# Performance work log

Hardware: AMD Instinct MI355X
Metric: run time of the kernel (lower is better)

Reference implementation:

```python
import jax, jax.numpy as jnp
import numpy as np
from jax import lax

K = 3      # kernel size
PAD = 1    # padding (stride=1, dilation=1, single offset group)


def _deform_conv2d(x, off, weight, bias):
    # x: [B,C,H,W], off: [B,2*K*K,H,W] (y,x per tap), weight: [O,C,K,K], bias: [O]
    B, C, H, W = x.shape
    KK = K * K
    off = off.reshape(B, KK, 2, H, W)
    off_y, off_x = off[:, :, 0], off[:, :, 1]          # [B,KK,H,W]

    kh = jnp.repeat(jnp.arange(K, dtype=x.dtype), K)   # [KK] tap row offsets
    kw = jnp.tile(jnp.arange(K, dtype=x.dtype), K)     # [KK] tap col offsets
    py = (jnp.arange(H, dtype=x.dtype)[None, None, :, None] - PAD
          + kh[None, :, None, None] + off_y)           # [B,KK,H,W] sample rows
    px = (jnp.arange(W, dtype=x.dtype)[None, None, None, :] - PAD
          + kw[None, :, None, None] + off_x)           # [B,KK,H,W] sample cols

    y0 = jnp.floor(py); x0 = jnp.floor(px)
    wy1 = py - y0; wx1 = px - x0
    wy0 = 1.0 - wy1; wx0 = 1.0 - wx1

    bidx = jnp.arange(B)[:, None, None, None]

    def gather(iy, ix):
        # zero outside the input (torchvision semantics)
        valid = (iy >= 0) & (iy < H) & (ix >= 0) & (ix < W)
        iyc = jnp.clip(iy, 0, H - 1).astype(jnp.int32)
        ixc = jnp.clip(ix, 0, W - 1).astype(jnp.int32)
        v = x[bidx, :, iyc, ixc]                       # [B,KK,H,W,C]
        return v * valid[..., None].astype(x.dtype)

    samp = (gather(y0, x0)           * (wy0 * wx0)[..., None]
            + gather(y0, x0 + 1)     * (wy0 * wx1)[..., None]
            + gather(y0 + 1, x0)     * (wy1 * wx0)[..., None]
            + gather(y0 + 1, x0 + 1) * (wy1 * wx1)[..., None])  # [B,KK,H,W,C]

    w = weight.reshape(weight.shape[0], C, KK)          # [O,C,KK]
    out = jnp.einsum('bkhwc,ock->bohw', samp, w) + bias[None, :, None, None]
    return out


def setup_inputs() -> dict:
    key = jax.random.key(0)
    k1, k2, k3 = jax.random.split(key, 3)
    B, C, O, H, W = 4, 64, 64, 128, 128
    x = jax.random.normal(k1, (B, C, H, W), dtype=jnp.float32)
    offset_w = jax.random.normal(k2, (2 * K * K, C, 3, 3), dtype=jnp.float32) * 0.02
    offset_b = jnp.zeros((2 * K * K,), dtype=jnp.float32)
    weight = jax.random.normal(k3, (O, C, K, K), dtype=jnp.float32) * 0.01
    bias = jnp.zeros((O,), dtype=jnp.float32)
    return {"x": x, "offset_w": offset_w, "offset_b": offset_b,
            "weight": weight, "bias": bias}


def reference(x, offset_w, offset_b, weight, bias):
    # offset-predicting conv (3x3, pad 1)
    off = lax.conv_general_dilated(
        x, offset_w, window_strides=(1, 1), padding='SAME',
        dimension_numbers=('NCHW', 'OIHW', 'NCHW')) + offset_b[None, :, None, None]
    return _deform_conv2d(x, off, weight, bias)
```

## Files before the change

### kernel.cpp

```cpp
#include <hip/hip_runtime.h>
#include <hip/hip_bf16.h>


typedef short short8 __attribute__((ext_vector_type(8)));
typedef short short4v __attribute__((ext_vector_type(4)));
typedef float f32x4 __attribute__((ext_vector_type(4)));

static __device__ inline short bf16s(float f) {
    __hip_bfloat16 h = __float2bfloat16(f);
    return *(short*)&h;
}
static __device__ inline float lo2f(unsigned u) { return __uint_as_float(u << 16); }
static __device__ inline float hi2f(unsigned u) { return __uint_as_float(u & 0xffff0000u); }

__global__ void prep_kernel(const float* __restrict__ offset_w,
                            const float* __restrict__ weight,
                            __hip_bfloat16* __restrict__ Wb,
                            __hip_bfloat16* __restrict__ OWb)
{
    int id = blockIdx.x * 256 + threadIdx.x;
    if (id < 36864) {
        int j    = id & 7;
        int lane = (id >> 3) & 63;
        int id3  = id >> 9;
        int s    = id3 % 18;
        int otile = id3 / 18;
        int n = lane & 15, q = lane >> 4;
        int kap = s * 32 + q * 8 + j;
        int k = kap >> 6, c = kap & 63;
        int o = otile * 16 + n;
        Wb[id] = __float2bfloat16(weight[(o * 64 + c) * 9 + k]);
    }
    int id2 = id - 36864;
    if (id2 >= 0 && id2 < 18432) {
        int j    = id2 & 7;
        int lane = (id2 >> 3) & 63;
        int id3  = id2 >> 9;
        int s    = id3 % 18;
        int ntile = id3 / 18;
        int n = lane & 15, q = lane >> 4;
        int kap = s * 32 + q * 8 + j;
        int k = kap >> 6, c = kap & 63;
        int o = ntile * 16 + n;
        float v = (o < 18) ? offset_w[(o * 64 + c) * 9 + k] : 0.0f;
        OWb[id2] = __float2bfloat16(v);
    }
}

__global__ void transpose_kernel(const float* __restrict__ x, __hip_bfloat16* __restrict__ xB)
{
    __shared__ __align__(16) float lds[128 * 65];
    int bh = blockIdx.x;
    int b = bh >> 7, h = bh & 127;
    int t = threadIdx.x;
    int w = t & 127, chalf = t >> 7;
    for (int i = 0; i < 32; ++i) {
        int c = i * 2 + chalf;
        lds[w * 65 + c] = x[((b * 64 + c) * 128 + h) * 128 + w];
    }
    __syncthreads();
    unsigned* dst = (unsigned*)(xB + ((b * 128 + h) * 128) * 64);
    for (int i = 0; i < 16; ++i) {
        int L = i * 256 + t;
        int ww = L >> 5, c2 = L & 31;
        float f0 = lds[ww * 65 + c2 * 2];
        float f1 = lds[ww * 65 + c2 * 2 + 1];
        unsigned pk = ((unsigned)bf16s(f0) & 0xffffu) | ((unsigned)bf16s(f1) << 16);
        dst[L] = pk;
    }
}

__global__ __launch_bounds__(256, 6) void deform_kernel(
    const __hip_bfloat16* __restrict__ xB,
    const __hip_bfloat16* __restrict__ Wb,
    const __hip_bfloat16* __restrict__ OWb,
    const float* __restrict__ offset_b,
    const float* __restrict__ bias,
    float* __restrict__ out)
{
    __shared__ __align__(16) short sampB[18 * 16 * 40];
    __shared__ __align__(16) float offL[288];

    int t = threadIdx.x, wv = t >> 6, lane = t & 63;
    int bid = blockIdx.x;
    int b  = bid >> 10;
    int h  = (bid >> 3) & 127;
    int w0 = (bid & 7) << 4;

    short* patch = sampB;

    {
        int c2 = t & 31, pg = t >> 5;
        const __hip_bfloat16* xbb = xB + b * (128 * 128 * 64) + c2 * 2;
#pragma unroll
        for (int i = 0; i < 7; ++i) {
            int pix = i * 8 + pg;
            if (pix < 54) {
                int row = pix / 18, col = pix - row * 18;
                int hh = h - 1 + row, ww2 = w0 - 1 + col;
                unsigned v = 0;
                if (hh >= 0 && hh < 128 && ww2 >= 0 && ww2 < 128)
                    v = *(const unsigned*)(xbb + (hh * 128 + ww2) * 64);
                *(unsigned*)&patch[pix * 80 + c2 * 2] = v;
            }
        }
    }
    __syncthreads();

    if (wv < 2) {
        int n = lane & 15, q = lane >> 4;
        const short8* Bw = (const short8*)OWb + (wv * 18) * 64 + lane;
        f32x4 acc = {0.f, 0.f, 0.f, 0.f};
#pragma unroll
        for (int s = 0; s < 18; ++s) {
            int k = s >> 1;
            int ky = k / 3, kx = k - ky * 3;
            int pix = ky * 18 + n + kx;
            const short8 a = *(const short8*)&patch[pix * 80 + (s & 1) * 32 + q * 8];
            acc = __builtin_amdgcn_mfma_f32_16x16x32_bf16(a, Bw[s * 64], acc, 0, 0, 0);
        }
        int o = wv * 16 + n;
        if (o < 18) {
            float bo = offset_b[o];
#pragma unroll
            for (int r = 0; r < 4; ++r)
                offL[o * 16 + q * 4 + r] = acc[r] + bo;
        }
    }
    __syncthreads();

    {
        int g = lane >> 4, c4 = lane & 15;
        int p = wv * 4 + g;
        const __hip_bfloat16* xb4 = xB + b * (128 * 128 * 64) + c4 * 4;

        float offy[9], offx[9];
#pragma unroll
        for (int k = 0; k < 9; ++k) {
            offy[k] = offL[(2 * k) * 16 + p];
            offx[k] = offL[(2 * k + 1) * 16 + p];
        }

#pragma unroll
        for (int k = 0; k < 9; ++k) {
            float py = (float)(h - 1 + (k / 3)) + offy[k];
            float px = (float)(w0 + p - 1 + (k % 3)) + offx[k];
            float y0f = floorf(py), x0f = floorf(px);
            float wy1 = py - y0f, wx1 = px - x0f;
            float wy0 = 1.0f - wy1, wx0 = 1.0f - wx1;
            int iy = (int)y0f, ix = (int)x0f;
            bool y0v = (iy >= 0) && (iy < 128);
            bool y1v = (iy >= -1) && (iy < 127);
            bool x0v = (ix >= 0) && (ix < 128);
            bool x1v = (ix >= -1) && (ix < 127);
            int iy0c = min(max(iy, 0), 127), iy1c = min(max(iy + 1, 0), 127);
            int ix0c = min(max(ix, 0), 127), ix1c = min(max(ix + 1, 0), 127);
            int e00 = (iy0c * 128 + ix0c) * 64;
            int e01 = (iy0c * 128 + ix1c) * 64;
            int e10 = (iy1c * 128 + ix0c) * 64;
            int e11 = (iy1c * 128 + ix1c) * 64;
            float wa = (y0v && x0v) ? wy0 * wx0 : 0.0f;
            float wb_ = (y0v && x1v) ? wy0 * wx1 : 0.0f;
            float wc = (y1v && x0v) ? wy1 * wx0 : 0.0f;
            float wd = (y1v && x1v) ? wy1 * wx1 : 0.0f;

            uint2 r0 = *(const uint2*)(xb4 + e00);
            uint2 r1 = *(const uint2*)(xb4 + e01);
            uint2 r2 = *(const uint2*)(xb4 + e10);
            uint2 r3 = *(const uint2*)(xb4 + e11);

            float s0 = fmaf(wd, lo2f(r3.x), fmaf(wc, lo2f(r2.x), fmaf(wb_, lo2f(r1.x), wa * lo2f(r0.x))));
            float s1 = fmaf(wd, hi2f(r3.x), fmaf(wc, hi2f(r2.x), fmaf(wb_, hi2f(r1.x), wa * hi2f(r0.x))));
            float s2 = fmaf(wd, lo2f(r3.y), fmaf(wc, lo2f(r2.y), fmaf(wb_, lo2f(r1.y), wa * lo2f(r0.y))));
            float s3 = fmaf(wd, hi2f(r3.y), fmaf(wc, hi2f(r2.y), fmaf(wb_, hi2f(r1.y), wa * hi2f(r0.y))));
            int s = 2 * k + (c4 >> 3);
            short4v pk = { bf16s(s0), bf16s(s1), bf16s(s2), bf16s(s3) };
            *(short4v*)&sampB[(s * 16 + p) * 40 + (c4 & 7) * 4] = pk;
        }
    }
    __syncthreads();

    {
        int n = lane & 15, q = lane >> 4;
        int arow = n * 40 + q * 8;
        const short8* BwW = (const short8*)Wb + (wv * 18) * 64 + lane;
        f32x4 acc = {0.f, 0.f, 0.f, 0.f};
#pragma unroll
        for (int s = 0; s < 18; ++s) {
            const short8 a = *(const short8*)&sampB[s * 640 + arow];
            acc = __builtin_amdgcn_mfma_f32_16x16x32_bf16(a, BwW[s * 64], acc, 0, 0, 0);
        }
        int o = wv * 16 + n;
        float bo = bias[o];
        float4 st = {acc[0] + bo, acc[1] + bo, acc[2] + bo, acc[3] + bo};
        *(float4*)&out[((b * 64 + o) * 128 + h) * 128 + w0 + q * 4] = st;
    }
}

extern "C" void kernel_launch(void* const* d_in, const int* in_sizes, int n_in,
                              void* d_out, int out_size, void* d_ws, size_t ws_size,
                              hipStream_t stream) {
    const float* x        = (const float*)d_in[0];
    const float* offset_w = (const float*)d_in[1];
    const float* offset_b = (const float*)d_in[2];
    const float* weight   = (const float*)d_in[3];
    const float* bias     = (const float*)d_in[4];
    char* ws = (char*)d_ws;
    __hip_bfloat16* xB  = (__hip_bfloat16*)ws;
    __hip_bfloat16* Wb  = (__hip_bfloat16*)(ws + 8388608);
    __hip_bfloat16* OWb = (__hip_bfloat16*)(ws + 8388608 + 73728);
    float* outp = (float*)d_out;

    hipLaunchKernelGGL(prep_kernel,      dim3(216),  dim3(256), 0, stream, offset_w, weight, Wb, OWb);
    hipLaunchKernelGGL(transpose_kernel, dim3(512),  dim3(256), 0, stream, x, xB);
    hipLaunchKernelGGL(deform_kernel,    dim3(4096), dim3(256), 0, stream, xB, Wb, OWb, offset_b, bias, outp);
}
```

Before: 115.3 us.

## Zero-pad bf16 input layout and split offset conv into its own kernel

The transposed bf16 input now has a one-pixel zero border (130x130), so the bilinear gather can clamp indices into the border instead of doing per-corner validity masks. The offset-predicting conv moves out of the deform kernel into a separate kernel that tiles 64 columns per block, uses all four waves, and writes the offsets to a global buffer. The deform kernel then only loads its 288 precomputed offsets. This trades an extra launch and a round trip of the offsets through global memory for less branch and index math and better MFMA utilisation in the offset conv.

```diff
diff --git a/kernel.cpp b/kernel.cpp
--- a/kernel.cpp
+++ b/kernel.cpp
@@ -47,19 +47,29 @@
     }
 }
 
-__global__ void transpose_kernel(const float* __restrict__ x, __hip_bfloat16* __restrict__ xB)
+__global__ void transpose_kernel(const float* __restrict__ x, __hip_bfloat16* __restrict__ xBp)
 {
     __shared__ __align__(16) float lds[128 * 65];
-    int bh = blockIdx.x;
-    int b = bh >> 7, h = bh & 127;
+    int blk = blockIdx.x;
+    int b = blk / 130, r = blk - b * 130;
     int t = threadIdx.x;
+    unsigned* rowp = (unsigned*)(xBp + (size_t)(b * 130 + r) * 130 * 64);
+    if (r == 0 || r == 129) {
+        uint4 z = {0u, 0u, 0u, 0u};
+        for (int i = 0; i < 5; ++i) {
+            int e = i * 256 + t;
+            if (e < 1040) ((uint4*)rowp)[e] = z;
+        }
+        return;
+    }
+    int h = r - 1;
     int w = t & 127, chalf = t >> 7;
     for (int i = 0; i < 32; ++i) {
         int c = i * 2 + chalf;
         lds[w * 65 + c] = x[((b * 64 + c) * 128 + h) * 128 + w];
     }
     __syncthreads();
-    unsigned* dst = (unsigned*)(xB + ((b * 128 + h) * 128) * 64);
+    unsigned* dst = rowp + 32;
     for (int i = 0; i < 16; ++i) {
         int L = i * 256 + t;
         int ww = L >> 5, c2 = L & 31;
@@ -68,13 +78,70 @@
         unsigned pk = ((unsigned)bf16s(f0) & 0xffffu) | ((unsigned)bf16s(f1) << 16);
         dst[L] = pk;
     }
-}
-
-__global__ __launch_bounds__(256, 6) void deform_kernel(
-    const __hip_bfloat16* __restrict__ xB,
-    const __hip_bfloat16* __restrict__ Wb,
+    if (t < 64) {
+        int col = (t >> 5) * 129;
+        rowp[col * 32 + (t & 31)] = 0u;
+    }
+}
+
+__global__ __launch_bounds__(256, 4) void offconv_kernel(
+    const __hip_bfloat16* __restrict__ xBp,
     const __hip_bfloat16* __restrict__ OWb,
     const float* __restrict__ offset_b,
+    float* __restrict__ off_g)
+{
+    __shared__ __align__(16) short patch[198 * 80];
+
+    int t = threadIdx.x, wv = t >> 6, lane = t & 63;
+    int bid = blockIdx.x;
+    int half = bid & 1;
+    int bh = bid >> 1;
+    int b = bh >> 7, h = bh & 127;
+    int w0 = half * 64;
+
+    for (int i = 0; i < 7; ++i) {
+        int e = i * 256 + t;
+        if (e < 1584) {
+            int px = e >> 3, part = e & 7;
+            int prow = px / 66, pcol = px - prow * 66;
+            const uint4* src = (const uint4*)(xBp +
+                (size_t)((b * 130 + h + prow) * 130 + w0 + pcol) * 64 + part * 8);
+            *(uint4*)&patch[px * 80 + part * 8] = *src;
+        }
+    }
+    __syncthreads();
+
+    int n = lane & 15, q = lane >> 4;
+    const short8* Bw = (const short8*)OWb;
+    f32x4 acc0 = {0.f, 0.f, 0.f, 0.f};
+    f32x4 acc1 = {0.f, 0.f, 0.f, 0.f};
+#pragma unroll
+    for (int s = 0; s < 18; ++s) {
+        int k = s >> 1;
+        int ky = k / 3, kx = k - ky * 3;
+        int pix = ky * 66 + wv * 16 + n + kx;
+        const short8 a = *(const short8*)&patch[pix * 80 + (s & 1) * 32 + q * 8];
+        acc0 = __builtin_amdgcn_mfma_f32_16x16x32_bf16(a, Bw[(0 * 18 + s) * 64 + lane], acc0, 0, 0, 0);
+        acc1 = __builtin_amdgcn_mfma_f32_16x16x32_bf16(a, Bw[(1 * 18 + s) * 64 + lane], acc1, 0, 0, 0);
+    }
+    float* og = off_g + ((size_t)(b * 128 + h) * 18) * 128 + w0 + wv * 16 + q * 4;
+    {
+        float bo = offset_b[n];
+        float4 st = {acc0[0] + bo, acc0[1] + bo, acc0[2] + bo, acc0[3] + bo};
+        *(float4*)&og[n * 128] = st;
+    }
+    if (n < 2) {
+        int o = 16 + n;
+        float bo = offset_b[o];
+        float4 st = {acc1[0] + bo, acc1[1] + bo, acc1[2] + bo, acc1[3] + bo};
+        *(float4*)&og[o * 128] = st;
+    }
+}
+
+__global__ __launch_bounds__(256, 6) void deform_kernel(
+    const __hip_bfloat16* __restrict__ xBp,
+    const __hip_bfloat16* __restrict__ Wb,
+    const float* __restrict__ off_g,
     const float* __restrict__ bias,
     float* __restrict__ out)
 {
@@ -87,52 +154,16 @@
     int h  = (bid >> 3) & 127;
     int w0 = (bid & 7) << 4;
 
-    short* patch = sampB;
-
-    {
-        int c2 = t & 31, pg = t >> 5;
-        const __hip_bfloat16* xbb = xB + b * (128 * 128 * 64) + c2 * 2;
-#pragma unroll
-        for (int i = 0; i < 7; ++i) {
-            int pix = i * 8 + pg;
-            if (pix < 54) {
-                int row = pix / 18, col = pix - row * 18;
-                int hh = h - 1 + row, ww2 = w0 - 1 + col;
-                unsigned v = 0;
-                if (hh >= 0 && hh < 128 && ww2 >= 0 && ww2 < 128)
-                    v = *(const unsigned*)(xbb + (hh * 128 + ww2) * 64);
-                *(unsigned*)&patch[pix * 80 + c2 * 2] = v;
-            }
-        }
-    }
-    __syncthreads();
-
-    if (wv < 2) {
-        int n = lane & 15, q = lane >> 4;
-        const short8* Bw = (const short8*)OWb + (wv * 18) * 64 + lane;
-        f32x4 acc = {0.f, 0.f, 0.f, 0.f};
-#pragma unroll
-        for (int s = 0; s < 18; ++s) {
-            int k = s >> 1;
-            int ky = k / 3, kx = k - ky * 3;
-            int pix = ky * 18 + n + kx;
-            const short8 a = *(const short8*)&patch[pix * 80 + (s & 1) * 32 + q * 8];
-            acc = __builtin_amdgcn_mfma_f32_16x16x32_bf16(a, Bw[s * 64], acc, 0, 0, 0);
-        }
-        int o = wv * 16 + n;
-        if (o < 18) {
-            float bo = offset_b[o];
-#pragma unroll
-            for (int r = 0; r < 4; ++r)
-                offL[o * 16 + q * 4 + r] = acc[r] + bo;
-        }
+    for (int e = t; e < 288; e += 256) {
+        int o = e >> 4, p = e & 15;
+        offL[o * 16 + p] = off_g[((size_t)((b * 128 + h) * 18 + o)) * 128 + w0 + p];
     }
     __syncthreads();
 
     {
         int g = lane >> 4, c4 = lane & 15;
         int p = wv * 4 + g;
-        const __hip_bfloat16* xb4 = xB + b * (128 * 128 * 64) + c4 * 4;
+        const __hip_bfloat16* xb4 = xBp + (size_t)b * (130 * 130 * 64) + c4 * 4 + 131 * 64;
 
         float offy[9], offx[9];
 #pragma unroll
@@ -149,20 +180,19 @@
             float wy1 = py - y0f, wx1 = px - x0f;
             float wy0 = 1.0f - wy1, wx0 = 1.0f - wx1;
             int iy = (int)y0f, ix = (int)x0f;
-            bool y0v = (iy >= 0) && (iy < 128);
-            bool y1v = (iy >= -1) && (iy < 127);
-            bool x0v = (ix >= 0) && (ix < 128);
-            bool x1v = (ix >= -1) && (ix < 127);
-            int iy0c = min(max(iy, 0), 127), iy1c = min(max(iy + 1, 0), 127);
-            int ix0c = min(max(ix, 0), 127), ix1c = min(max(ix + 1, 0), 127);
-            int e00 = (iy0c * 128 + ix0c) * 64;
-            int e01 = (iy0c * 128 + ix1c) * 64;
-            int e10 = (iy1c * 128 + ix0c) * 64;
-            int e11 = (iy1c * 128 + ix1c) * 64;
-            float wa = (y0v && x0v) ? wy0 * wx0 : 0.0f;
-            float wb_ = (y0v && x1v) ? wy0 * wx1 : 0.0f;
-            float wc = (y1v && x0v) ? wy1 * wx0 : 0.0f;
-            float wd = (y1v && x1v) ? wy1 * wx1 : 0.0f;
+            int iy0 = min(max(iy, -1), 128);
+            int ix0 = min(max(ix, -1), 128);
+            int iy1 = min(max(iy + 1, -1), 128);
+            int ix1 = min(max(ix + 1, -1), 128);
+            int rb0 = iy0 * 130, rb1 = iy1 * 130;
+            int e00 = (rb0 + ix0) * 64;
+            int e01 = (rb0 + ix1) * 64;
+            int e10 = (rb1 + ix0) * 64;
+            int e11 = (rb1 + ix1) * 64;
+            float wa  = wy0 * wx0;
+            float wb_ = wy0 * wx1;
+            float wc  = wy1 * wx0;
+            float wd  = wy1 * wx1;
 
             uint2 r0 = *(const uint2*)(xb4 + e00);
             uint2 r1 = *(const uint2*)(xb4 + e01);
@@ -193,7 +223,7 @@
         int o = wv * 16 + n;
         float bo = bias[o];
         float4 st = {acc[0] + bo, acc[1] + bo, acc[2] + bo, acc[3] + bo};
-        *(float4*)&out[((b * 64 + o) * 128 + h) * 128 + w0 + q * 4] = st;
+        *(float4*)&out[(((size_t)b * 64 + o) * 128 + h) * 128 + w0 + q * 4] = st;
     }
 }
 
@@ -206,12 +236,14 @@
     const float* weight   = (const float*)d_in[3];
     const float* bias     = (const float*)d_in[4];
     char* ws = (char*)d_ws;
-    __hip_bfloat16* xB  = (__hip_bfloat16*)ws;
-    __hip_bfloat16* Wb  = (__hip_bfloat16*)(ws + 8388608);
-    __hip_bfloat16* OWb = (__hip_bfloat16*)(ws + 8388608 + 73728);
+    __hip_bfloat16* xBp = (__hip_bfloat16*)ws;
+    __hip_bfloat16* Wb  = (__hip_bfloat16*)(ws + 8652800);
+    __hip_bfloat16* OWb = (__hip_bfloat16*)(ws + 8652800 + 73728);
+    float* off_g        = (float*)(ws + 8652800 + 73728 + 36864);
     float* outp = (float*)d_out;
 
     hipLaunchKernelGGL(prep_kernel,      dim3(216),  dim3(256), 0, stream, offset_w, weight, Wb, OWb);
-    hipLaunchKernelGGL(transpose_kernel, dim3(512),  dim3(256), 0, stream, x, xB);
-    hipLaunchKernelGGL(deform_kernel,    dim3(4096), dim3(256), 0, stream, xB, Wb, OWb, offset_b, bias, outp);
-}
+    hipLaunchKernelGGL(transpose_kernel, dim3(520),  dim3(256), 0, stream, x, xBp);
+    hipLaunchKernelGGL(offconv_kernel,   dim3(1024), dim3(256), 0, stream, xBp, OWb, offset_b, off_g);
+    hipLaunchKernelGGL(deform_kernel,    dim3(4096), dim3(256), 0, stream, xBp, Wb, off_g, bias, outp);
+}
```

Measured after the change: 120.3 us. 4.3% more time.
